# Kernel tuning notes

Measured on AMD Instinct MI355X. Metric: run time of the kernel, lower is better.

The kernel has to match this reference:

```python
import jax, jax.numpy as jnp
import numpy as np

B = 32; H = 56; W = 56; C = 384; NH = 12; WS = 7; SS = 3
N = WS * WS            # tokens per window = 49
NW = (H // WS) * (W // WS)  # windows per image = 64
HD = C // NH           # head dim = 32
MLP_H = 4 * C
EPS = 1e-5


def _rel_pos_index():
    coords = np.stack(np.meshgrid(np.arange(WS), np.arange(WS), indexing='ij'))
    cf = coords.reshape(2, -1)                      # (2, N)
    rel = cf[:, :, None] - cf[:, None, :]           # (2, N, N)
    rel = rel.transpose(1, 2, 0).astype(np.int64)   # (N, N, 2)
    rel[..., 0] += WS - 1
    rel[..., 1] += WS - 1
    rel[..., 0] *= 2 * WS - 1
    return rel.sum(-1)                               # (N, N)


def _attn_mask():
    img = np.zeros((H, W))
    cnt = 0
    slc = (slice(0, -WS), slice(-WS, -SS), slice(-SS, None))
    for hs in slc:
        for ws in slc:
            img[hs, ws] = cnt
            cnt += 1
    mw = img.reshape(H // WS, WS, W // WS, WS).transpose(0, 2, 1, 3).reshape(-1, N)  # (NW, N)
    diff = mw[:, None, :] - mw[:, :, None]
    return np.where(diff != 0, -100.0, 0.0).astype(np.float32)  # (NW, N, N)


_RPI = jnp.asarray(_rel_pos_index())
_MASK = jnp.asarray(_attn_mask())


def _ln(x, w, b):
    m = jnp.mean(x, axis=-1, keepdims=True)
    v = jnp.mean((x - m) ** 2, axis=-1, keepdims=True)
    return (x - m) * jax.lax.rsqrt(v + EPS) * w + b


def _window_partition(x):  # (B,H,W,C) -> (B*NW, WS, WS, C)
    x = x.reshape(B, H // WS, WS, W // WS, WS, C)
    return x.transpose(0, 1, 3, 2, 4, 5).reshape(-1, WS, WS, C)


def _window_reverse(xw):  # (B*NW, WS, WS, C) -> (B,H,W,C)
    x = xw.reshape(B, H // WS, W // WS, WS, WS, C)
    return x.transpose(0, 1, 3, 2, 4, 5).reshape(B, H, W, C)


def setup_inputs() -> dict:
    key = jax.random.key(0)
    ks = jax.random.split(key, 8)
    s = 0.02
    return {
        'x': jax.random.normal(ks[0], (B, H * W, C), jnp.float32),
        'norm1_w': jnp.ones((C,), jnp.float32),
        'norm1_b': jnp.zeros((C,), jnp.float32),
        'qkv_w': jax.random.normal(ks[1], (C, 3 * C), jnp.float32) * s,
        'qkv_b': jnp.zeros((3 * C,), jnp.float32),
        'rpb_table': jax.random.normal(ks[2], ((2 * WS - 1) * (2 * WS - 1), NH), jnp.float32) * s,
        'proj_w': jax.random.normal(ks[3], (C, C), jnp.float32) * s,
        'proj_b': jnp.zeros((C,), jnp.float32),
        'norm2_w': jnp.ones((C,), jnp.float32),
        'norm2_b': jnp.zeros((C,), jnp.float32),
        'fc1_w': jax.random.normal(ks[4], (C, MLP_H), jnp.float32) * s,
        'fc1_b': jnp.zeros((MLP_H,), jnp.float32),
        'fc2_w': jax.random.normal(ks[5], (MLP_H, C), jnp.float32) * s,
        'fc2_b': jnp.zeros((C,), jnp.float32),
    }


def reference(x, norm1_w, norm1_b, qkv_w, qkv_b, rpb_table, proj_w, proj_b,
              norm2_w, norm2_b, fc1_w, fc1_b, fc2_w, fc2_b):
    shortcut = x
    xn = _ln(x, norm1_w, norm1_b).reshape(B, H, W, C)
    # cyclic shift
    xs = jnp.roll(xn, shift=(-SS, -SS), axis=(1, 2))
    xw = _window_partition(xs).reshape(-1, N, C)           # (B*NW, N, C)

    qkv = (xw @ qkv_w + qkv_b).reshape(-1, N, 3, NH, HD)
    qkv = qkv.transpose(2, 0, 3, 1, 4)                      # (3, B*NW, NH, N, HD)
    q, k, v = qkv[0], qkv[1], qkv[2]
    q = q * (HD ** -0.5)
    attn = jnp.einsum('bhnd,bhmd->bhnm', q, k)              # (B*NW, NH, N, N)

    bias = rpb_table[_RPI.reshape(-1)].reshape(N, N, NH).transpose(2, 0, 1)
    attn = attn + bias[None]
    # shift mask: (NW, N, N) broadcast over batch and heads
    attn = attn.reshape(B, NW, NH, N, N) + _MASK[None, :, None]
    attn = jax.nn.softmax(attn.reshape(-1, NH, N, N), axis=-1)

    out = jnp.einsum('bhnm,bhmd->bhnd', attn, v)            # (B*NW, NH, N, HD)
    out = out.transpose(0, 2, 1, 3).reshape(-1, N, C)
    out = out @ proj_w + proj_b

    out = _window_reverse(out.reshape(-1, WS, WS, C))
    out = jnp.roll(out, shift=(SS, SS), axis=(1, 2)).reshape(B, H * W, C)

    x = shortcut + out
    h = _ln(x, norm2_w, norm2_b)
    h = jax.nn.gelu(h @ fc1_w + fc1_b, approximate=False) @ fc2_w + fc2_b
    return x + h
```

## Files before the change

### kernel.cpp

```cpp
#include <hip/hip_runtime.h>
#include <hip/hip_bf16.h>
#include <math.h>


typedef short bf16x8 __attribute__((ext_vector_type(8)));
typedef float f32x4 __attribute__((ext_vector_type(4)));

__global__ __launch_bounds__(256) void prep_k(
    const float* __restrict__ qkvw, const float* __restrict__ projw,
    const float* __restrict__ fc1w, const float* __restrict__ fc2w,
    const float* __restrict__ rpb,
    __hip_bfloat16* __restrict__ wt_qkv, __hip_bfloat16* __restrict__ wt_proj,
    __hip_bfloat16* __restrict__ wt_fc1, __hip_bfloat16* __restrict__ wt_fc2,
    float* __restrict__ biasM) {
    int id = blockIdx.x * 256 + threadIdx.x;
    if (id < 442368) {
        int k = id / 1152, n = id % 1152;
        wt_qkv[(size_t)n * 384 + k] = __float2bfloat16(qkvw[id]);
        return;
    }
    id -= 442368;
    if (id < 147456) {
        int k = id / 384, n = id % 384;
        wt_proj[(size_t)n * 384 + k] = __float2bfloat16(projw[id]);
        return;
    }
    id -= 147456;
    if (id < 589824) {
        int k = id / 1536, n = id % 1536;
        wt_fc1[(size_t)n * 384 + k] = __float2bfloat16(fc1w[id]);
        return;
    }
    id -= 589824;
    if (id < 589824) {
        int k = id / 384, n = id % 384;
        wt_fc2[(size_t)n * 1536 + k] = __float2bfloat16(fc2w[id]);
        return;
    }
    id -= 589824;
    if (id < 28812) {
        int h = id / 2401, rem = id % 2401, i = rem / 49, j = rem % 49;
        int ih = i / 7, iw = i % 7, jh = j / 7, jw = j % 7;
        int idx = (ih - jh + 6) * 13 + (iw - jw + 6);
        biasM[id] = rpb[idx * 12 + h];
    }
}

template <int MODE>
__global__ __launch_bounds__(256) void ln_k(const float* __restrict__ X,
                                            const float* __restrict__ w,
                                            const float* __restrict__ b,
                                            __hip_bfloat16* __restrict__ out) {
    int wv = threadIdx.x >> 6, lane = threadIdx.x & 63;
    int row = blockIdx.x * 4 + wv;
    size_t src_row;
    if (MODE == 0) {
        int wi = row / 49, t = row % 49;
        int bb = wi >> 6, wrem = wi & 63;
        int wh = wrem >> 3, ww = wrem & 7;
        int th = t / 7, tw = t % 7;
        int hi = (wh * 7 + th + 3) % 56;
        int wimg = (ww * 7 + tw + 3) % 56;
        src_row = (size_t)(bb * 3136 + hi * 56 + wimg);
    } else {
        src_row = row;
    }
    const float* src = X + src_row * 384;
    float v[6];
    float s = 0.f, sq = 0.f;
#pragma unroll
    for (int i = 0; i < 6; i++) {
        v[i] = src[lane + i * 64];
        s += v[i];
        sq += v[i] * v[i];
    }
#pragma unroll
    for (int m = 32; m >= 1; m >>= 1) {
        s += __shfl_xor(s, m, 64);
        sq += __shfl_xor(sq, m, 64);
    }
    float mean = s * (1.f / 384.f);
    float var = sq * (1.f / 384.f) - mean * mean;
    float rstd = rsqrtf(var + 1e-5f);
    size_t orow = (size_t)row * 384;
#pragma unroll
    for (int i = 0; i < 6; i++) {
        int c = lane + i * 64;
        out[orow + c] = __float2bfloat16((v[i] - mean) * rstd * w[c] + b[c]);
    }
}

template <int EPI>
__global__ __launch_bounds__(256, 2) void gemm_k(
    const __hip_bfloat16* __restrict__ A, const __hip_bfloat16* __restrict__ Bt,
    const float* __restrict__ bias, int K, int nTilesN,
    __hip_bfloat16* outb, float* outf, const float* resin) {
    __shared__ __align__(16) __hip_bfloat16 lb[2][128 * 64];
    int bid = blockIdx.x;
    bid = (bid & 7) * ((int)gridDim.x >> 3) + (bid >> 3);
    int tM = bid / nTilesN, tN = bid % nTilesN;
    size_t m0 = (size_t)tM * 128;
    int n0 = tN * 128;
    int tid = threadIdx.x, wv = tid >> 6, lane = tid & 63;
    int lm = lane & 15, lg = lane >> 4;

    f32x4 acc[2][8];
#pragma unroll
    for (int m = 0; m < 2; m++)
#pragma unroll
        for (int j = 0; j < 8; j++) acc[m][j] = (f32x4){0.f, 0.f, 0.f, 0.f};

    const __hip_bfloat16* pA = A + (m0 + wv * 32 + lm) * K + lg * 8;
    int brow = tid >> 1;
    const __hip_bfloat16* pB = Bt + (size_t)(n0 + brow) * K + (tid & 1) * 32;
    int wof[4];
#pragma unroll
    for (int i = 0; i < 4; i++)
        wof[i] = brow * 64 + ((((tid & 1) * 4 + i) ^ (brow & 7)) * 8);
    int rof0 = ((0 + lg) ^ (lm & 7)) * 8;
    int rof1 = ((4 + lg) ^ (lm & 7)) * 8;

    int nkt = K >> 6;

    bf16x8 bst[4];
    bf16x8 aA[2][2], aB[2][2];

#define LOADB(T)                                                               \
    do {                                                                       \
        const __hip_bfloat16* p_ = pB + (size_t)(T) * 64;                      \
        bst[0] = *(const bf16x8*)(p_);                                         \
        bst[1] = *(const bf16x8*)(p_ + 8);                                     \
        bst[2] = *(const bf16x8*)(p_ + 16);                                    \
        bst[3] = *(const bf16x8*)(p_ + 24);                                    \
    } while (0)
#define LOADA(DST, T)                                                          \
    do {                                                                       \
        const __hip_bfloat16* p_ = pA + (size_t)(T) * 64;                      \
        DST[0][0] = *(const bf16x8*)(p_);                                      \
        DST[0][1] = *(const bf16x8*)(p_ + 32);                                 \
        DST[1][0] = *(const bf16x8*)(p_ + (size_t)16 * K);                     \
        DST[1][1] = *(const bf16x8*)(p_ + (size_t)16 * K + 32);                \
    } while (0)
#define WRITEB(P)                                                              \
    do {                                                                       \
        *(bf16x8*)&lb[P][wof[0]] = bst[0];                                     \
        *(bf16x8*)&lb[P][wof[1]] = bst[1];                                     \
        *(bf16x8*)&lb[P][wof[2]] = bst[2];                                     \
        *(bf16x8*)&lb[P][wof[3]] = bst[3];                                     \
    } while (0)
#define COMPUTE(P, AC)                                                         \
    do {                                                                       \
        _Pragma("unroll") for (int j = 0; j < 8; j++) {                        \
            bf16x8 b0 = *(const bf16x8*)&lb[P][(j * 16 + lm) * 64 + rof0];     \
            bf16x8 b1 = *(const bf16x8*)&lb[P][(j * 16 + lm) * 64 + rof1];     \
            acc[0][j] = __builtin_amdgcn_mfma_f32_16x16x32_bf16(               \
                AC[0][0], b0, acc[0][j], 0, 0, 0);                             \
            acc[0][j] = __builtin_amdgcn_mfma_f32_16x16x32_bf16(               \
                AC[0][1], b1, acc[0][j], 0, 0, 0);                             \
            acc[1][j] = __builtin_amdgcn_mfma_f32_16x16x32_bf16(               \
                AC[1][0], b0, acc[1][j], 0, 0, 0);                             \
            acc[1][j] = __builtin_amdgcn_mfma_f32_16x16x32_bf16(               \
                AC[1][1], b1, acc[1][j], 0, 0, 0);                             \
        }                                                                      \
    } while (0)
#define ENDBAR()                                                               \
    do {                                                                       \
        asm volatile("s_waitcnt lgkmcnt(0)" ::: "memory");                     \
        __builtin_amdgcn_sched_barrier(0);                                     \
        __builtin_amdgcn_s_barrier();                                          \
        __builtin_amdgcn_sched_barrier(0);                                     \
    } while (0)
#define ITER(P, AC, T)                                                         \
    do {                                                                       \
        if ((T) + 1 < nkt) WRITEB(P ^ 1);                                      \
        if ((T) + 2 < nkt) LOADB((T) + 2);                                     \
        COMPUTE(P, AC);                                                        \
        if ((T) + 2 < nkt) LOADA(AC, (T) + 2);                                 \
        ENDBAR();                                                              \
    } while (0)

    LOADB(0);
    LOADA(aA, 0);
    WRITEB(0);
    LOADB(1);
    LOADA(aB, 1);
    ENDBAR();

    for (int t = 0; t < nkt; t += 2) {
        ITER(0, aA, t);
        ITER(1, aB, t + 1);
    }
#undef ITER
#undef ENDBAR
#undef COMPUTE
#undef WRITEB
#undef LOADA
#undef LOADB

    int ld = nTilesN * 128;
#pragma unroll
    for (int m = 0; m < 2; m++) {
#pragma unroll
        for (int r = 0; r < 4; r++) {
            int row = (int)m0 + wv * 32 + m * 16 + lg * 4 + r;
#pragma unroll
            for (int j = 0; j < 8; j++) {
                int col = n0 + j * 16 + lm;
                float val = acc[m][j][r] + bias[col];
                if (EPI == 0) {
                    outb[(size_t)row * ld + col] = __float2bfloat16(val);
                } else if (EPI == 2) {
                    float g = 0.5f * val * (1.f + erff(val * 0.70710678118f));
                    outb[(size_t)row * ld + col] = __float2bfloat16(g);
                } else if (EPI == 1) {
                    int wi = row / 49, t = row % 49;
                    int bb = wi >> 6, wrem = wi & 63;
                    int wh = wrem >> 3, ww = wrem & 7;
                    int th = t / 7, tw = t % 7;
                    int hi = (wh * 7 + th + 3) % 56;
                    int wimg = (ww * 7 + tw + 3) % 56;
                    size_t pos = (size_t)(bb * 3136 + hi * 56 + wimg) * 384 + col;
                    outf[pos] = resin[pos] + val;
                } else {
                    size_t pos = (size_t)row * 384 + col;
                    outf[pos] = resin[pos] + val;
                }
            }
        }
    }
}

__global__ __launch_bounds__(256) void attn_k(const __hip_bfloat16* __restrict__ qkv,
                                              const float* __restrict__ biasM,
                                              __hip_bfloat16* __restrict__ out) {
    __shared__ __align__(16) __hip_bfloat16 vt[32 * 72];
    __shared__ __align__(16) __hip_bfloat16 P[64 * 72];
    int bid = blockIdx.x;
    bid = (bid & 7) * ((int)gridDim.x >> 3) + (bid >> 3);
    int wi = bid / 12, h = bid % 12;
    int tid = threadIdx.x, wv = tid >> 6, lane = tid & 63;
    int lm = lane & 15, lg = lane >> 4;
    int wrem = wi & 63, wh = wrem >> 3, ww = wrem & 7;

#pragma unroll
    for (int i = 0; i < 9; i++) vt[tid * 9 + i] = __float2bfloat16(0.f);
    __syncthreads();
    if (tid < 196) {
        int t = tid >> 2, d0 = (tid & 3) * 8;
        bf16x8 vv = *(const bf16x8*)(qkv + (size_t)(wi * 49 + t) * 1152 + 768 + h * 32 + d0);
#pragma unroll
        for (int i = 0; i < 8; i++) vt[(d0 + i) * 72 + t] = ((__hip_bfloat16*)&vv)[i];
    }

    int qrow = wv * 16 + lm;
    if (qrow > 48) qrow = 48;
    bf16x8 aq = *(const bf16x8*)(qkv + (size_t)(wi * 49 + qrow) * 1152 + h * 32 + lg * 8);
    f32x4 S[4];
#pragma unroll
    for (int ct = 0; ct < 4; ct++) {
        int krow = ct * 16 + lm;
        if (krow > 48) krow = 48;
        bf16x8 bk = *(const bf16x8*)(qkv + (size_t)(wi * 49 + krow) * 1152 + 384 + h * 32 + lg * 8);
        S[ct] = __builtin_amdgcn_mfma_f32_16x16x32_bf16(aq, bk, (f32x4){0.f, 0.f, 0.f, 0.f}, 0, 0, 0);
    }

    const float scale = 0.17677669529663687f;
#pragma unroll
    for (int r = 0; r < 4; r++) {
        int irow = wv * 16 + lg * 4 + r;
        int ic = irow <= 48 ? irow : 48;
        int ith = ic / 7, itw = ic % 7;
        int ihs = wh * 7 + ith, iws = ww * 7 + itw;
        int ridi = (ihs < 49 ? 0 : (ihs < 53 ? 1 : 2)) * 3 + (iws < 49 ? 0 : (iws < 53 ? 1 : 2));
        float vals[4];
        float mx = -1e30f;
#pragma unroll
        for (int ct = 0; ct < 4; ct++) {
            int jcol = ct * 16 + lm;
            float sv;
            if (jcol < 49) {
                int jth = jcol / 7, jtw = jcol % 7;
                int jhs = wh * 7 + jth, jws = ww * 7 + jtw;
                int ridj = (jhs < 49 ? 0 : (jhs < 53 ? 1 : 2)) * 3 + (jws < 49 ? 0 : (jws < 53 ? 1 : 2));
                sv = S[ct][r] * scale + biasM[h * 2401 + ic * 49 + jcol] +
                     (ridi != ridj ? -100.f : 0.f);
            } else {
                sv = -1e30f;
            }
            vals[ct] = sv;
            mx = fmaxf(mx, sv);
        }
#pragma unroll
        for (int m = 8; m >= 1; m >>= 1) mx = fmaxf(mx, __shfl_xor(mx, m, 64));
        float sum = 0.f;
#pragma unroll
        for (int ct = 0; ct < 4; ct++) {
            vals[ct] = __expf(vals[ct] - mx);
            sum += vals[ct];
        }
#pragma unroll
        for (int m = 8; m >= 1; m >>= 1) sum += __shfl_xor(sum, m, 64);
        float inv = 1.f / sum;
#pragma unroll
        for (int ct = 0; ct < 4; ct++)
            P[irow * 72 + ct * 16 + lm] = __float2bfloat16(vals[ct] * inv);
    }
    __syncthreads();

    f32x4 O[2] = {{0.f, 0.f, 0.f, 0.f}, {0.f, 0.f, 0.f, 0.f}};
#pragma unroll
    for (int ks = 0; ks < 2; ks++) {
        bf16x8 ap = *(const bf16x8*)&P[(wv * 16 + lm) * 72 + ks * 32 + lg * 8];
#pragma unroll
        for (int nt = 0; nt < 2; nt++) {
            bf16x8 bv = *(const bf16x8*)&vt[(nt * 16 + lm) * 72 + ks * 32 + lg * 8];
            O[nt] = __builtin_amdgcn_mfma_f32_16x16x32_bf16(ap, bv, O[nt], 0, 0, 0);
        }
    }
#pragma unroll
    for (int r = 0; r < 4; r++) {
        int row = wv * 16 + lg * 4 + r;
        if (row < 49) {
            size_t base = (size_t)(wi * 49 + row) * 384 + h * 32;
            out[base + lm] = __float2bfloat16(O[0][r]);
            out[base + 16 + lm] = __float2bfloat16(O[1][r]);
        }
    }
}

extern "C" void kernel_launch(void* const* d_in, const int* in_sizes, int n_in,
                              void* d_out, int out_size, void* d_ws, size_t ws_size,
                              hipStream_t stream) {
    (void)in_sizes; (void)n_in; (void)out_size; (void)ws_size;
    const float* x     = (const float*)d_in[0];
    const float* n1w   = (const float*)d_in[1];
    const float* n1b   = (const float*)d_in[2];
    const float* qkvw  = (const float*)d_in[3];
    const float* qkvb  = (const float*)d_in[4];
    const float* rpb   = (const float*)d_in[5];
    const float* projw = (const float*)d_in[6];
    const float* projb = (const float*)d_in[7];
    const float* n2w   = (const float*)d_in[8];
    const float* n2b   = (const float*)d_in[9];
    const float* fc1w  = (const float*)d_in[10];
    const float* fc1b  = (const float*)d_in[11];
    const float* fc2w  = (const float*)d_in[12];
    const float* fc2b  = (const float*)d_in[13];
    float* out = (float*)d_out;

    char* ws = (char*)d_ws;
    __hip_bfloat16* wt_qkv  = (__hip_bfloat16*)(ws + 0);
    __hip_bfloat16* wt_proj = (__hip_bfloat16*)(ws + 884736);
    __hip_bfloat16* wt_fc1  = (__hip_bfloat16*)(ws + 1179648);
    __hip_bfloat16* wt_fc2  = (__hip_bfloat16*)(ws + 2359296);
    float*          biasM   = (float*)(ws + 3538944);
    __hip_bfloat16* xw      = (__hip_bfloat16*)(ws + 3654656);
    __hip_bfloat16* qkv     = (__hip_bfloat16*)(ws + 80724992);
    __hip_bfloat16* attn_o  = (__hip_bfloat16*)(ws + 311936000);
    __hip_bfloat16* hidden  = xw;
    __hip_bfloat16* hn      = attn_o;

    prep_k<<<7025, 256, 0, stream>>>(qkvw, projw, fc1w, fc2w, rpb,
                                     wt_qkv, wt_proj, wt_fc1, wt_fc2, biasM);

    ln_k<0><<<25088, 256, 0, stream>>>(x, n1w, n1b, xw);
    gemm_k<0><<<784 * 9, 256, 0, stream>>>(xw, wt_qkv, qkvb, 384, 9, qkv, nullptr, nullptr);
    attn_k<<<2048 * 12, 256, 0, stream>>>(qkv, biasM, attn_o);
    gemm_k<1><<<784 * 3, 256, 0, stream>>>(attn_o, wt_proj, projb, 384, 3, nullptr, out, x);
    ln_k<1><<<25088, 256, 0, stream>>>(out, n2w, n2b, hn);
    gemm_k<2><<<784 * 12, 256, 0, stream>>>(hn, wt_fc1, fc1b, 384, 12, hidden, nullptr, nullptr);
    gemm_k<3><<<784 * 3, 256, 0, stream>>>(hidden, wt_fc2, fc2b, 1536, 3, nullptr, out, out);
}
```

Measured before the change: 1.309 ms.

## Widen GEMM tiles to 128x384 with 16-wave blocks staging A and B in LDS

The GEMM kernel moves from 256-thread blocks computing 128x128 tiles to 1024-thread blocks computing 128x384 tiles, arranged as a 4x4 grid of waves each owning 32x96. Both A and B tiles are now staged in shared memory with an XOR swizzle, where before A was read directly from global memory into registers. The intent is to cut redundant A reads across N tiles and raise arithmetic intensity per block. In exchange it uses more LDS (128 KB for the double buffer), launches far fewer blocks, and puts a larger barrier cost on a 1024-thread block. The launch_bounds of (1024, 4) looks unreachable given the LDS size.

New measurement: 1.204 ms. 8.0% less time.

```diff
diff --git a/kernel.cpp b/kernel.cpp
--- a/kernel.cpp
+++ b/kernel.cpp
@@ -91,76 +91,73 @@
 }
 
 template <int EPI>
-__global__ __launch_bounds__(256, 2) void gemm_k(
+__global__ __launch_bounds__(1024, 4) void gemm_k(
     const __hip_bfloat16* __restrict__ A, const __hip_bfloat16* __restrict__ Bt,
     const float* __restrict__ bias, int K, int nTilesN,
     __hip_bfloat16* outb, float* outf, const float* resin) {
-    __shared__ __align__(16) __hip_bfloat16 lb[2][128 * 64];
+    __shared__ __align__(16) __hip_bfloat16 lb[2][(128 + 384) * 64];
     int bid = blockIdx.x;
     bid = (bid & 7) * ((int)gridDim.x >> 3) + (bid >> 3);
     int tM = bid / nTilesN, tN = bid % nTilesN;
     size_t m0 = (size_t)tM * 128;
-    int n0 = tN * 128;
+    int n0 = tN * 384;
     int tid = threadIdx.x, wv = tid >> 6, lane = tid & 63;
+    int wr = wv >> 2, wc = wv & 3;
     int lm = lane & 15, lg = lane >> 4;
 
-    f32x4 acc[2][8];
+    f32x4 acc[2][6];
 #pragma unroll
     for (int m = 0; m < 2; m++)
 #pragma unroll
-        for (int j = 0; j < 8; j++) acc[m][j] = (f32x4){0.f, 0.f, 0.f, 0.f};
-
-    const __hip_bfloat16* pA = A + (m0 + wv * 32 + lm) * K + lg * 8;
-    int brow = tid >> 1;
-    const __hip_bfloat16* pB = Bt + (size_t)(n0 + brow) * K + (tid & 1) * 32;
-    int wof[4];
-#pragma unroll
-    for (int i = 0; i < 4; i++)
-        wof[i] = brow * 64 + ((((tid & 1) * 4 + i) ^ (brow & 7)) * 8);
-    int rof0 = ((0 + lg) ^ (lm & 7)) * 8;
-    int rof1 = ((4 + lg) ^ (lm & 7)) * 8;
+        for (int j = 0; j < 6; j++) acc[m][j] = (f32x4){0.f, 0.f, 0.f, 0.f};
+
+    int row0 = tid >> 3, c0 = tid & 7;
+    const __hip_bfloat16* gA = A + (m0 + row0) * K + c0 * 8;
+    const __hip_bfloat16* gB = Bt + (size_t)(n0 + row0) * K + c0 * 8;
+    int wofA = row0 * 64 + ((c0 ^ (row0 & 7)) * 8);
+    int wofB = 8192 + wofA;
+
+    int rsw0 = ((0 + lg) ^ (lm & 7)) * 8;
+    int rsw1 = ((4 + lg) ^ (lm & 7)) * 8;
+    int arow = (wr * 32 + lm) * 64;
+    int brow = 8192 + (wc * 96 + lm) * 64;
 
     int nkt = K >> 6;
 
-    bf16x8 bst[4];
-    bf16x8 aA[2][2], aB[2][2];
-
-#define LOADB(T)                                                               \
-    do {                                                                       \
-        const __hip_bfloat16* p_ = pB + (size_t)(T) * 64;                      \
-        bst[0] = *(const bf16x8*)(p_);                                         \
-        bst[1] = *(const bf16x8*)(p_ + 8);                                     \
-        bst[2] = *(const bf16x8*)(p_ + 16);                                    \
-        bst[3] = *(const bf16x8*)(p_ + 24);                                    \
-    } while (0)
-#define LOADA(DST, T)                                                          \
-    do {                                                                       \
-        const __hip_bfloat16* p_ = pA + (size_t)(T) * 64;                      \
-        DST[0][0] = *(const bf16x8*)(p_);                                      \
-        DST[0][1] = *(const bf16x8*)(p_ + 32);                                 \
-        DST[1][0] = *(const bf16x8*)(p_ + (size_t)16 * K);                     \
-        DST[1][1] = *(const bf16x8*)(p_ + (size_t)16 * K + 32);                \
-    } while (0)
-#define WRITEB(P)                                                              \
-    do {                                                                       \
-        *(bf16x8*)&lb[P][wof[0]] = bst[0];                                     \
-        *(bf16x8*)&lb[P][wof[1]] = bst[1];                                     \
-        *(bf16x8*)&lb[P][wof[2]] = bst[2];                                     \
-        *(bf16x8*)&lb[P][wof[3]] = bst[3];                                     \
-    } while (0)
-#define COMPUTE(P, AC)                                                         \
-    do {                                                                       \
-        _Pragma("unroll") for (int j = 0; j < 8; j++) {                        \
-            bf16x8 b0 = *(const bf16x8*)&lb[P][(j * 16 + lm) * 64 + rof0];     \
-            bf16x8 b1 = *(const bf16x8*)&lb[P][(j * 16 + lm) * 64 + rof1];     \
+    bf16x8 st[4];
+
+#define LOADT(T)                                                               \
+    do {                                                                       \
+        size_t k0_ = (size_t)(T) * 64;                                         \
+        st[0] = *(const bf16x8*)(gA + k0_);                                    \
+        st[1] = *(const bf16x8*)(gB + k0_);                                    \
+        st[2] = *(const bf16x8*)(gB + (size_t)128 * K + k0_);                  \
+        st[3] = *(const bf16x8*)(gB + (size_t)256 * K + k0_);                  \
+    } while (0)
+#define WRITET(P)                                                              \
+    do {                                                                       \
+        *(bf16x8*)&lb[P][wofA] = st[0];                                        \
+        *(bf16x8*)&lb[P][wofB] = st[1];                                        \
+        *(bf16x8*)&lb[P][wofB + 8192] = st[2];                                 \
+        *(bf16x8*)&lb[P][wofB + 16384] = st[3];                                \
+    } while (0)
+#define COMPUTE(P)                                                             \
+    do {                                                                       \
+        bf16x8 af00 = *(const bf16x8*)&lb[P][arow + rsw0];                     \
+        bf16x8 af01 = *(const bf16x8*)&lb[P][arow + rsw1];                     \
+        bf16x8 af10 = *(const bf16x8*)&lb[P][arow + 1024 + rsw0];              \
+        bf16x8 af11 = *(const bf16x8*)&lb[P][arow + 1024 + rsw1];              \
+        _Pragma("unroll") for (int j = 0; j < 6; j++) {                        \
+            bf16x8 b0 = *(const bf16x8*)&lb[P][brow + j * 1024 + rsw0];        \
+            bf16x8 b1 = *(const bf16x8*)&lb[P][brow + j * 1024 + rsw1];        \
             acc[0][j] = __builtin_amdgcn_mfma_f32_16x16x32_bf16(               \
-                AC[0][0], b0, acc[0][j], 0, 0, 0);                             \
+                af00, b0, acc[0][j], 0, 0, 0);                                 \
+            acc[1][j] = __builtin_amdgcn_mfma_f32_16x16x32_bf16(               \
+                af10, b0, acc[1][j], 0, 0, 0);                                 \
             acc[0][j] = __builtin_amdgcn_mfma_f32_16x16x32_bf16(               \
-                AC[0][1], b1, acc[0][j], 0, 0, 0);                             \
+                af01, b1, acc[0][j], 0, 0, 0);                                 \
             acc[1][j] = __builtin_amdgcn_mfma_f32_16x16x32_bf16(               \
-                AC[1][0], b0, acc[1][j], 0, 0, 0);                             \
-            acc[1][j] = __builtin_amdgcn_mfma_f32_16x16x32_bf16(               \
-                AC[1][1], b1, acc[1][j], 0, 0, 0);                             \
+                af11, b1, acc[1][j], 0, 0, 0);                                 \
         }                                                                      \
     } while (0)
 #define ENDBAR()                                                               \
@@ -170,42 +167,38 @@
         __builtin_amdgcn_s_barrier();                                          \
         __builtin_amdgcn_sched_barrier(0);                                     \
     } while (0)
-#define ITER(P, AC, T)                                                         \
-    do {                                                                       \
-        if ((T) + 1 < nkt) WRITEB(P ^ 1);                                      \
-        if ((T) + 2 < nkt) LOADB((T) + 2);                                     \
-        COMPUTE(P, AC);                                                        \
-        if ((T) + 2 < nkt) LOADA(AC, (T) + 2);                                 \
+#define ITER(P, T)                                                             \
+    do {                                                                       \
+        if ((T) + 1 < nkt) WRITET(P ^ 1);                                      \
+        if ((T) + 2 < nkt) LOADT((T) + 2);                                     \
+        COMPUTE(P);                                                            \
         ENDBAR();                                                              \
     } while (0)
 
-    LOADB(0);
-    LOADA(aA, 0);
-    WRITEB(0);
-    LOADB(1);
-    LOADA(aB, 1);
+    LOADT(0);
+    WRITET(0);
+    LOADT(1);
     ENDBAR();
 
     for (int t = 0; t < nkt; t += 2) {
-        ITER(0, aA, t);
-        ITER(1, aB, t + 1);
+        ITER(0, t);
+        ITER(1, t + 1);
     }
 #undef ITER
 #undef ENDBAR
 #undef COMPUTE
-#undef WRITEB
-#undef LOADA
-#undef LOADB
-
-    int ld = nTilesN * 128;
+#undef WRITET
+#undef LOADT
+
+    int ld = nTilesN * 384;
 #pragma unroll
     for (int m = 0; m < 2; m++) {
 #pragma unroll
         for (int r = 0; r < 4; r++) {
-            int row = (int)m0 + wv * 32 + m * 16 + lg * 4 + r;
-#pragma unroll
-            for (int j = 0; j < 8; j++) {
-                int col = n0 + j * 16 + lm;
+            int row = (int)m0 + wr * 32 + m * 16 + lg * 4 + r;
+#pragma unroll
+            for (int j = 0; j < 6; j++) {
+                int col = n0 + wc * 96 + j * 16 + lm;
                 float val = acc[m][j][r] + bias[col];
                 if (EPI == 0) {
                     outb[(size_t)row * ld + col] = __float2bfloat16(val);
@@ -364,10 +357,10 @@
                                      wt_qkv, wt_proj, wt_fc1, wt_fc2, biasM);
 
     ln_k<0><<<25088, 256, 0, stream>>>(x, n1w, n1b, xw);
-    gemm_k<0><<<784 * 9, 256, 0, stream>>>(xw, wt_qkv, qkvb, 384, 9, qkv, nullptr, nullptr);
+    gemm_k<0><<<784 * 3, 1024, 0, stream>>>(xw, wt_qkv, qkvb, 384, 3, qkv, nullptr, nullptr);
     attn_k<<<2048 * 12, 256, 0, stream>>>(qkv, biasM, attn_o);
-    gemm_k<1><<<784 * 3, 256, 0, stream>>>(attn_o, wt_proj, projb, 384, 3, nullptr, out, x);
+    gemm_k<1><<<784, 1024, 0, stream>>>(attn_o, wt_proj, projb, 384, 1, nullptr, out, x);
     ln_k<1><<<25088, 256, 0, stream>>>(out, n2w, n2b, hn);
-    gemm_k<2><<<784 * 12, 256, 0, stream>>>(hn, wt_fc1, fc1b, 384, 12, hidden, nullptr, nullptr);
-    gemm_k<3><<<784 * 3, 256, 0, stream>>>(hidden, wt_fc2, fc2b, 1536, 3, nullptr, out, out);
-}
+    gemm_k<2><<<784 * 4, 1024, 0, stream>>>(hn, wt_fc1, fc1b, 384, 4, hidden, nullptr, nullptr);
+    gemm_k<3><<<784, 1024, 0, stream>>>(hidden, wt_fc2, fc2b, 1536, 1, nullptr, out, out);
+}
```
